# Optimization experiments

Hardware: AMD Instinct MI355X
Metric: run time of the kernel (lower is better)

The kernel has to match this reference:

```python
import jax, jax.numpy as jnp
import numpy as np

BIG = 1.0e9   # sentinel for masked distances / masked max
K_NBR = 64    # max_num_neighbors in radius()


def _fps(pos, n_sample):
    """Farthest point sampling on a single cloud pos [N, D] -> int32 [n_sample]."""
    n = pos.shape[0]

    def body(i, st):
        d, idxs = st
        last = pos[idxs[i - 1]]                              # [D]
        d = jnp.minimum(d, jnp.sum((pos - last) ** 2, axis=-1))
        return d, idxs.at[i].set(jnp.argmax(d).astype(jnp.int32))

    d0 = jnp.full((n,), BIG, pos.dtype)
    idxs0 = jnp.zeros((n_sample,), jnp.int32)
    _, idxs = jax.lax.fori_loop(1, n_sample, body, (d0, idxs0))
    return idxs


def _mlp2(h, w1, b1, w2, b2):
    # PyG MLP([a,b,c]) in eval mode (dropout off, batch-norm at default running
    # stats == identity): Linear -> ReLU -> Linear (plain last layer).
    return jax.nn.relu(h @ w1 + b1) @ w2 + b2


_gather = jax.vmap(lambda a, i: a[i])  # per-cloud fancy gather


def _sa(x, pos, ratio, r, w1, b1, w2, b2):
    """SAModule: FPS -> radius neighbors (<=K) -> PointConv (gather, MLP on
    [x_j, pos_j - pos_i], max-aggregate). Dense batched: x [B,N,C], pos [B,N,D]."""
    B, N, D = pos.shape
    M = int(round(N * ratio))
    idx = jax.vmap(lambda p: _fps(p, M))(pos)                 # [B, M]
    pos_q = _gather(pos, idx)                                 # [B, M, D]
    # pairwise squared distances query -> all points  [B, M, N]
    d2 = jnp.sum((pos_q[:, :, None, :] - pos[:, None, :, :]) ** 2, axis=-1)
    neg = jnp.where(d2 <= r * r, -d2, -BIG)
    vals, nbr = jax.lax.top_k(neg, K_NBR)                     # [B, M, K]
    valid = vals > -0.5 * BIG                                 # in-radius mask
    x_j = _gather(x, nbr)                                     # [B, M, K, C]
    rel = _gather(pos, nbr) - pos_q[:, :, None, :]            # [B, M, K, D]
    h = _mlp2(jnp.concatenate([x_j, rel], axis=-1), w1, b1, w2, b2)
    h = jnp.where(valid[..., None], h, -BIG)
    return jnp.max(h, axis=2), pos_q                          # max aggregation


def setup_inputs() -> dict:
    key = jax.random.key(0)
    ks = jax.random.split(key, 12)
    B, N, D, F = 8, 4096, 2, 5

    def lin(k, fi, fo):
        return (jax.random.normal(k, (fi, fo), jnp.float32) / np.sqrt(fi)).astype(jnp.float32)

    return {
        "x": jax.random.normal(ks[0], (B, N, F), jnp.float32),
        "pos": jax.random.uniform(ks[1], (B, N, D), jnp.float32),
        # sa1: MLP([5+2, 32, 64])
        "w1a": lin(ks[2], 7, 32),   "b1a": jnp.zeros((32,), jnp.float32),
        "w1b": lin(ks[3], 32, 64),  "b1b": jnp.zeros((64,), jnp.float32),
        # sa2: MLP([64+2, 64, 128])
        "w2a": lin(ks[4], 66, 64),  "b2a": jnp.zeros((64,), jnp.float32),
        "w2b": lin(ks[5], 64, 128), "b2b": jnp.zeros((128,), jnp.float32),
        # sa3 (global): MLP([128+2, 128, 256])
        "w3a": lin(ks[6], 130, 128), "b3a": jnp.zeros((128,), jnp.float32),
        "w3b": lin(ks[7], 128, 256), "b3b": jnp.zeros((256,), jnp.float32),
        # head: MLP([256, 256, 1024], norm=None)
        "w4a": lin(ks[8], 256, 256),  "b4a": jnp.zeros((256,), jnp.float32),
        "w4b": lin(ks[9], 256, 1024), "b4b": jnp.zeros((1024,), jnp.float32),
    }


def reference(x, pos, w1a, b1a, w1b, b1b, w2a, b2a, w2b, b2b,
              w3a, b3a, w3b, b3b, w4a, b4a, w4b, b4b):
    h1, p1 = _sa(x, pos, 0.5, 0.2, w1a, b1a, w1b, b1b)       # [B, N/2, 64]
    h2, p2 = _sa(h1, p1, 0.25, 0.4, w2a, b2a, w2b, b2b)      # [B, N/8, 128]
    g = _mlp2(jnp.concatenate([h2, p2], axis=-1), w3a, b3a, w3b, b3b)
    g = jnp.max(g, axis=1)                                    # global max pool [B, 256]
    return _mlp2(g, w4a, b4a, w4b, b4b)                       # [B, 1024]
```

## Files before the change

kernel.cpp:

```cpp
#include <hip/hip_runtime.h>


template<int N, int T>
__global__ __launch_bounds__(T) void fps_kernel(
    const float* __restrict__ pos,
    float* __restrict__ posq,
    int M) {
  constexpr int PPT = N / T;
  constexpr int NW  = T / 64;
  __shared__ float sx[N], sy[N];
  __shared__ unsigned long long sp[2][NW];
  const int b = blockIdx.x, t = threadIdx.x;
  const float* p = pos + (size_t)b * N * 2;
  float x[PPT], y[PPT], d[PPT];
  {
    const float4* p4 = (const float4*)(p + (size_t)t * PPT * 2);
#pragma unroll
    for (int q = 0; q < PPT / 2; ++q) {
      float4 v = p4[q];
      x[2 * q + 0] = v.x; y[2 * q + 0] = v.y;
      x[2 * q + 1] = v.z; y[2 * q + 1] = v.w;
    }
  }
#pragma unroll
  for (int k = 0; k < PPT; ++k) {
    int pt = t * PPT + k;
    sx[pt] = x[k]; sy[pt] = y[k];
    d[k] = 1e9f;
  }
  __syncthreads();
  float lx = sx[0], ly = sy[0];
  if (t == 0) { posq[(size_t)b * M * 2 + 0] = lx; posq[(size_t)b * M * 2 + 1] = ly; }

#define DPP_UMAX(u, ctrl)                                                      \
  do {                                                                         \
    unsigned _o = (unsigned)__builtin_amdgcn_update_dpp(0, (int)(u), (ctrl),   \
                                                        0xf, 0xf, true);       \
    (u) = ((u) > _o) ? (u) : _o;                                               \
  } while (0)

  for (int i = 1; i < M; ++i) {
    float bv = -1.0f; int bp = 0;
#pragma unroll
    for (int k = 0; k < PPT; ++k) {
      float dx = x[k] - lx, dy = y[k] - ly;
      float dd = __fadd_rn(__fmul_rn(dx, dx), __fmul_rn(dy, dy));
      float nd = fminf(d[k], dd);
      d[k] = nd;
      if (nd > bv) { bv = nd; bp = t * PPT + k; }
    }
    const unsigned mybits = __float_as_uint(bv);
    unsigned u = mybits;
    DPP_UMAX(u, 0x111);
    DPP_UMAX(u, 0x112);
    DPP_UMAX(u, 0x114);
    DPP_UMAX(u, 0x118);
    DPP_UMAX(u, 0x142);
    DPP_UMAX(u, 0x143);
    const unsigned wvb = (unsigned)__builtin_amdgcn_readlane((int)u, 63);
    const unsigned long long tm = __ballot(mybits == wvb);
    const int fl = (int)__builtin_ctzll(tm);
    const int wbp = __builtin_amdgcn_readlane(bp, fl);

    const int par = i & 1;
    if ((t & 63) == 0)
      sp[par][t >> 6] = ((unsigned long long)wvb << 32) | (unsigned)(~wbp);
    __syncthreads();
    unsigned long long best = sp[par][0];
#pragma unroll
    for (int j = 1; j < NW; ++j) {
      unsigned long long v = sp[par][j];
      best = (v > best) ? v : best;
    }
    const int wi = (int)(~(unsigned)best);
    lx = sx[wi]; ly = sy[wi];
    if (t == 0) {
      posq[((size_t)b * M + i) * 2 + 0] = lx;
      posq[((size_t)b * M + i) * 2 + 1] = ly;
    }
  }
#undef DPP_UMAX
}

template<int CPL>
__global__ __launch_bounds__(256) void nbr_kernel(
    const float* __restrict__ pts,
    const float* __restrict__ posq,
    int* __restrict__ nbr,
    int M, int NPTS, int total_q, float R2) {
  const int wid = blockIdx.x * 4 + (threadIdx.x >> 6);
  if (wid >= total_q) return;
  const int lane = threadIdx.x & 63;
  const int b = wid / M;
  const float qx = posq[(size_t)wid * 2 + 0], qy = posq[(size_t)wid * 2 + 1];
  const float* p = pts + (size_t)b * NPTS * 2;
  unsigned bits[CPL];
  int cnt = 0;
#pragma unroll
  for (int k = 0; k < CPL; ++k) {
    int pt = lane + (k << 6);
    float dx = p[pt * 2 + 0] - qx, dy = p[pt * 2 + 1] - qy;
    float dd = __fadd_rn(__fmul_rn(dx, dx), __fmul_rn(dy, dy));
    bool inr = (dd <= R2);
    bits[k] = inr ? __float_as_uint(dd) : 0xFFFFFFFFu;
    cnt += __popcll(__ballot(inr));
  }
  const unsigned long long below = (1ULL << lane) - 1ULL;
  if (cnt <= 64) {
    int base = 0;
#pragma unroll
    for (int k = 0; k < CPL; ++k) {
      bool s = (bits[k] != 0xFFFFFFFFu);
      unsigned long long m = __ballot(s);
      if (s) nbr[(size_t)wid * 64 + base + __popcll(m & below)] = lane + (k << 6);
      base += __popcll(m);
    }
    for (int j = base + lane; j < 64; j += 64) nbr[(size_t)wid * 64 + j] = -1;
  } else {
    unsigned lo = 0, hi = __float_as_uint(R2);
    while (lo < hi) {
      unsigned mid = lo + ((hi - lo) >> 1);
      int c = 0;
#pragma unroll
      for (int k = 0; k < CPL; ++k) c += __popcll(__ballot(bits[k] <= mid));
      if (c >= 64) hi = mid; else lo = mid + 1;
    }
    int cless = 0;
#pragma unroll
    for (int k = 0; k < CPL; ++k) cless += __popcll(__ballot(bits[k] < lo));
    const int need = 64 - cless;
    int base = 0, tiecnt = 0;
#pragma unroll
    for (int k = 0; k < CPL; ++k) {
      bool tie = (bits[k] == lo);
      unsigned long long tm = __ballot(tie);
      bool s = (bits[k] < lo) || (tie && (tiecnt + __popcll(tm & below)) < need);
      tiecnt += __popcll(tm);
      unsigned long long m = __ballot(s);
      if (s) nbr[(size_t)wid * 64 + base + __popcll(m & below)] = lane + (k << 6);
      base += __popcll(m);
    }
  }
}

template<int CIN, int H, int COUT, int QPB, int NPTS, int HS, int W1P>
__global__ __launch_bounds__(64 * QPB) void conv_kernel(
    const float* __restrict__ x,
    const float* __restrict__ pts,
    const float* __restrict__ posq,
    const int* __restrict__ nbr,
    const float* __restrict__ W1, const float* __restrict__ b1,
    const float* __restrict__ W2, const float* __restrict__ b2,
    float* __restrict__ out,
    int M) {
  constexpr int CI2 = CIN + 2;
  __shared__ float sW1t[H * W1P];
  __shared__ float sB1[H];
  __shared__ float sHH[QPB * 64 * HS];
  const int tid = threadIdx.x;
  for (int j = tid; j < CI2 * H; j += 64 * QPB) {
    int c = j / H, h = j - c * H;
    sW1t[h * W1P + c] = W1[j];
  }
  for (int j = tid; j < H; j += 64 * QPB) sB1[j] = b1[j];
  __syncthreads();
  const int wv = tid >> 6, lane = tid & 63;
  const int wid = blockIdx.x * QPB + wv;
  const int b = wid / M;
  const int idx = nbr[(size_t)wid * 64 + lane];
  const unsigned long long vm = __ballot(idx >= 0);
  const int ii = (idx < 0) ? 0 : idx;
  float in[CI2];
  {
    const float* xp = x + ((size_t)b * NPTS + ii) * CIN;
#pragma unroll
    for (int c = 0; c < CIN; ++c) in[c] = xp[c];
    float qx = posq[(size_t)wid * 2 + 0], qy = posq[(size_t)wid * 2 + 1];
    const float* pp = pts + ((size_t)b * NPTS + ii) * 2;
    in[CIN] = pp[0] - qx;
    in[CIN + 1] = pp[1] - qy;
  }
  float* hbase = &sHH[wv * 64 * HS];
#pragma unroll
  for (int h = 0; h < H; h += 4) {
    float vv[4];
#pragma unroll
    for (int j = 0; j < 4; ++j) {
      float a = sB1[h + j];
#pragma unroll
      for (int c = 0; c < CI2; ++c) a = fmaf(in[c], sW1t[(h + j) * W1P + c], a);
      vv[j] = fmaxf(a, 0.0f);
    }
    *(float4*)&hbase[lane * HS + h] = make_float4(vv[0], vv[1], vv[2], vv[3]);
  }
#pragma unroll
  for (int half = 0; half < COUT / 64; ++half) {
    const int o = half * 64 + lane;
    float w2r[H];
#pragma unroll
    for (int h = 0; h < H; ++h) w2r[h] = W2[h * COUT + o];
    const float b2o = b2[o];
    float m = -1e30f;
    for (int n = 0; n < 64; ++n) {
      const float4* hp = (const float4*)&hbase[n * HS];
      float a = b2o;
#pragma unroll
      for (int j = 0; j < H / 4; ++j) {
        float4 hv = hp[j];
        a = fmaf(hv.x, w2r[4 * j + 0], a);
        a = fmaf(hv.y, w2r[4 * j + 1], a);
        a = fmaf(hv.z, w2r[4 * j + 2], a);
        a = fmaf(hv.w, w2r[4 * j + 3], a);
      }
      a = ((vm >> n) & 1ULL) ? a : -1e9f;
      m = fmaxf(m, a);
    }
    out[(size_t)wid * COUT + o] = m;
  }
}

__global__ __launch_bounds__(256) void u_kernel(
    const float* __restrict__ h2,
    const float* __restrict__ posq2,
    const float* __restrict__ W3a, const float* __restrict__ b3a,
    float* __restrict__ u) {
  const int p = blockIdx.x * 2 + (threadIdx.x >> 7);
  const int h = threadIdx.x & 127;
  const float* hp = h2 + (size_t)p * 128;
  float a = b3a[h];
  for (int c = 0; c < 128; ++c) a = fmaf(hp[c], W3a[c * 128 + h], a);
  a = fmaf(posq2[(size_t)p * 2 + 0], W3a[128 * 128 + h], a);
  a = fmaf(posq2[(size_t)p * 2 + 1], W3a[129 * 128 + h], a);
  u[(size_t)p * 128 + h] = fmaxf(a, 0.0f);
}

__global__ __launch_bounds__(256) void g_kernel(
    const float* __restrict__ u,
    const float* __restrict__ W3b, const float* __restrict__ b3b,
    float* __restrict__ part) {
  __shared__ float su[64 * 128];
  const int bb = blockIdx.x;
  const float* up = u + (size_t)bb * 64 * 128;
  for (int j = threadIdx.x; j < 64 * 128; j += 256) su[j] = up[j];
  __syncthreads();
  const int o = threadIdx.x;
  float w[128];
#pragma unroll
  for (int h = 0; h < 128; ++h) w[h] = W3b[h * 256 + o];
  float m = -1e30f;
  for (int p = 0; p < 64; ++p) {
    float a = b3b[o];
    const float4* sp = (const float4*)&su[p * 128];
#pragma unroll
    for (int j = 0; j < 32; ++j) {
      float4 v = sp[j];
      a = fmaf(v.x, w[4 * j + 0], a);
      a = fmaf(v.y, w[4 * j + 1], a);
      a = fmaf(v.z, w[4 * j + 2], a);
      a = fmaf(v.w, w[4 * j + 3], a);
    }
    m = fmaxf(m, a);
  }
  part[(size_t)bb * 256 + o] = m;
}

__global__ __launch_bounds__(256) void head_kernel(
    const float* __restrict__ part,
    const float* __restrict__ W4a, const float* __restrict__ b4a,
    const float* __restrict__ W4b, const float* __restrict__ b4b,
    float* __restrict__ out) {
  __shared__ float g[256], h4[256];
  const int b = blockIdx.x, t = threadIdx.x;
  float m = part[(size_t)(b * 8 + 0) * 256 + t];
  for (int c = 1; c < 8; ++c) m = fmaxf(m, part[(size_t)(b * 8 + c) * 256 + t]);
  g[t] = m;
  __syncthreads();
  float a = b4a[t];
  for (int c = 0; c < 256; ++c) a = fmaf(g[c], W4a[c * 256 + t], a);
  h4[t] = fmaxf(a, 0.0f);
  __syncthreads();
  for (int jj = 0; jj < 4; ++jj) {
    int o = t + jj * 256;
    float a2 = b4b[o];
    for (int c = 0; c < 256; ++c) a2 = fmaf(h4[c], W4b[c * 1024 + o], a2);
    out[(size_t)b * 1024 + o] = a2;
  }
}

extern "C" void kernel_launch(void* const* d_in, const int* in_sizes, int n_in,
                              void* d_out, int out_size, void* d_ws, size_t ws_size,
                              hipStream_t stream) {
  (void)in_sizes; (void)n_in; (void)out_size; (void)ws_size;
  const float* x   = (const float*)d_in[0];
  const float* pos = (const float*)d_in[1];
  const float* w1a = (const float*)d_in[2];  const float* b1a = (const float*)d_in[3];
  const float* w1b = (const float*)d_in[4];  const float* b1b = (const float*)d_in[5];
  const float* w2a = (const float*)d_in[6];  const float* b2a = (const float*)d_in[7];
  const float* w2b = (const float*)d_in[8];  const float* b2b = (const float*)d_in[9];
  const float* w3a = (const float*)d_in[10]; const float* b3a = (const float*)d_in[11];
  const float* w3b = (const float*)d_in[12]; const float* b3b = (const float*)d_in[13];
  const float* w4a = (const float*)d_in[14]; const float* b4a = (const float*)d_in[15];
  const float* w4b = (const float*)d_in[16]; const float* b4b = (const float*)d_in[17];
  float* outp = (float*)d_out;

  char* ws = (char*)d_ws;
  size_t off = 0;
  float* posq1 = (float*)(ws + off); off += (size_t)8 * 2048 * 2 * 4;
  float* posq2 = (float*)(ws + off); off += (size_t)8 * 512 * 2 * 4;
  int*   nbr1  = (int*)  (ws + off); off += (size_t)16384 * 64 * 4;
  int*   nbr2  = (int*)  (ws + off); off += (size_t)4096 * 64 * 4;
  float* h1    = (float*)(ws + off); off += (size_t)16384 * 64 * 4;
  float* h2    = (float*)(ws + off); off += (size_t)4096 * 128 * 4;
  float* u3    = (float*)(ws + off); off += (size_t)4096 * 128 * 4;
  float* part  = (float*)(ws + off); off += (size_t)64 * 256 * 4;

  fps_kernel<4096, 512><<<dim3(8), dim3(512), 0, stream>>>(pos, posq1, 2048);
  fps_kernel<2048, 512><<<dim3(8), dim3(512), 0, stream>>>(posq1, posq2, 512);
  nbr_kernel<64><<<dim3(4096), dim3(256), 0, stream>>>(pos, posq1, nbr1,
                                                       2048, 4096, 16384, 0.04f);
  conv_kernel<5, 32, 64, 4, 4096, 36, 8><<<dim3(4096), dim3(256), 0, stream>>>(
      x, pos, posq1, nbr1, w1a, b1a, w1b, b1b, h1, 2048);
  nbr_kernel<32><<<dim3(1024), dim3(256), 0, stream>>>(posq1, posq2, nbr2,
                                                       512, 2048, 4096, 0.16f);
  conv_kernel<64, 64, 128, 2, 2048, 68, 68><<<dim3(2048), dim3(128), 0, stream>>>(
      h1, posq1, posq2, nbr2, w2a, b2a, w2b, b2b, h2, 512);
  u_kernel<<<dim3(2048), dim3(256), 0, stream>>>(h2, posq2, w3a, b3a, u3);
  g_kernel<<<dim3(64), dim3(256), 0, stream>>>(u3, w3b, b3b, part);
  head_kernel<<<dim3(8), dim3(256), 0, stream>>>(part, w4a, b4a, w4b, b4b, outp);
}
```

Baseline: 1.995 ms.

## Fuse both FPS stages into one kernel and carry winner coordinates in reduction slots

Runs both farthest-point-sampling stages in a single kernel, keeping the sampled points in shared memory so the second stage skips a kernel launch and a global round trip. The winning point's coordinates now travel with its key in the per-wave shared slots and are picked out of registers with a select tree, which removes the dependent shared-memory lookup of the winner after each barrier. The per-thread argmax is split into two interleaved chains to shorten the dependency chain. The cost is more registers for the coordinate copies and a wider uint4 slot reduction done by every thread.

```diff
diff --git a/kernel.cpp b/kernel.cpp
--- a/kernel.cpp
+++ b/kernel.cpp
@@ -1,36 +1,5 @@
 #include <hip/hip_runtime.h>
 
-
-template<int N, int T>
-__global__ __launch_bounds__(T) void fps_kernel(
-    const float* __restrict__ pos,
-    float* __restrict__ posq,
-    int M) {
-  constexpr int PPT = N / T;
-  constexpr int NW  = T / 64;
-  __shared__ float sx[N], sy[N];
-  __shared__ unsigned long long sp[2][NW];
-  const int b = blockIdx.x, t = threadIdx.x;
-  const float* p = pos + (size_t)b * N * 2;
-  float x[PPT], y[PPT], d[PPT];
-  {
-    const float4* p4 = (const float4*)(p + (size_t)t * PPT * 2);
-#pragma unroll
-    for (int q = 0; q < PPT / 2; ++q) {
-      float4 v = p4[q];
-      x[2 * q + 0] = v.x; y[2 * q + 0] = v.y;
-      x[2 * q + 1] = v.z; y[2 * q + 1] = v.w;
-    }
-  }
-#pragma unroll
-  for (int k = 0; k < PPT; ++k) {
-    int pt = t * PPT + k;
-    sx[pt] = x[k]; sy[pt] = y[k];
-    d[k] = 1e9f;
-  }
-  __syncthreads();
-  float lx = sx[0], ly = sy[0];
-  if (t == 0) { posq[(size_t)b * M * 2 + 0] = lx; posq[(size_t)b * M * 2 + 1] = ly; }
 
 #define DPP_UMAX(u, ctrl)                                                      \
   do {                                                                         \
@@ -39,15 +8,58 @@
     (u) = ((u) > _o) ? (u) : _o;                                               \
   } while (0)
 
-  for (int i = 1; i < M; ++i) {
-    float bv = -1.0f; int bp = 0;
+__device__ __forceinline__ uint4 kmax4(uint4 a, uint4 b) {
+  unsigned long long ka = ((unsigned long long)a.y << 32) | a.x;
+  unsigned long long kb = ((unsigned long long)b.y << 32) | b.x;
+  bool c = kb > ka;
+  uint4 r;
+  r.x = c ? b.x : a.x; r.y = c ? b.y : a.y;
+  r.z = c ? b.z : a.z; r.w = c ? b.w : a.w;
+  return r;
+}
+
+template<int PPT, int T>
+__device__ __forceinline__ void fps_stage(
+    float (&xr)[PPT], float (&yr)[PPT], int Msel, int t,
+    float* wlx, float* wly, uint4* slots ) {
+  constexpr int NW = T / 64;
+  if (t == 0) { wlx[0] = xr[0]; wly[0] = yr[0]; }
+  __syncthreads();
+  float lx = wlx[0], ly = wly[0];
+  float d[PPT];
+#pragma unroll
+  for (int k = 0; k < PPT; ++k) d[k] = 1e9f;
+
+  for (int i = 1; i < Msel; ++i) {
+    float nd[PPT];
 #pragma unroll
     for (int k = 0; k < PPT; ++k) {
-      float dx = x[k] - lx, dy = y[k] - ly;
+      float dx = xr[k] - lx, dy = yr[k] - ly;
       float dd = __fadd_rn(__fmul_rn(dx, dx), __fmul_rn(dy, dy));
-      float nd = fminf(d[k], dd);
-      d[k] = nd;
-      if (nd > bv) { bv = nd; bp = t * PPT + k; }
+      float v = fminf(d[k], dd);
+      d[k] = v; nd[k] = v;
+    }
+    constexpr int HP = PPT / 2;
+    float bvA = nd[0]; int bkA = 0;
+    float bvB = nd[HP]; int bkB = HP;
+#pragma unroll
+    for (int k = 1; k < HP; ++k) {
+      if (nd[k] > bvA)      { bvA = nd[k];      bkA = k; }
+      if (nd[HP + k] > bvB) { bvB = nd[HP + k]; bkB = HP + k; }
+    }
+    float bv = bvA; int bk = bkA;
+    if (bvB > bvA) { bv = bvB; bk = bkB; }
+    float tx[PPT], ty[PPT];
+#pragma unroll
+    for (int k = 0; k < PPT; ++k) { tx[k] = xr[k]; ty[k] = yr[k]; }
+#pragma unroll
+    for (int s = 1; s < PPT; s <<= 1) {
+      bool c = (bk & s) != 0;
+#pragma unroll
+      for (int k = 0; k < PPT; k += 2 * s) {
+        tx[k] = c ? tx[k + s] : tx[k];
+        ty[k] = c ? ty[k + s] : ty[k];
+      }
     }
     const unsigned mybits = __float_as_uint(bv);
     unsigned u = mybits;
@@ -58,28 +70,63 @@
     DPP_UMAX(u, 0x142);
     DPP_UMAX(u, 0x143);
     const unsigned wvb = (unsigned)__builtin_amdgcn_readlane((int)u, 63);
-    const unsigned long long tm = __ballot(mybits == wvb);
-    const int fl = (int)__builtin_ctzll(tm);
-    const int wbp = __builtin_amdgcn_readlane(bp, fl);
-
+    const unsigned long long tmask = __ballot(mybits == wvb);
+    const int fl = (int)__builtin_ctzll(tmask);
     const int par = i & 1;
-    if ((t & 63) == 0)
-      sp[par][t >> 6] = ((unsigned long long)wvb << 32) | (unsigned)(~wbp);
+    if ((t & 63) == fl) {
+      uint4 s4;
+      s4.x = ~(unsigned)(t * PPT + bk);
+      s4.y = wvb;
+      s4.z = __float_as_uint(tx[0]);
+      s4.w = __float_as_uint(ty[0]);
+      slots[par * NW + (t >> 6)] = s4;
+    }
     __syncthreads();
-    unsigned long long best = sp[par][0];
-#pragma unroll
-    for (int j = 1; j < NW; ++j) {
-      unsigned long long v = sp[par][j];
-      best = (v > best) ? v : best;
-    }
-    const int wi = (int)(~(unsigned)best);
-    lx = sx[wi]; ly = sy[wi];
-    if (t == 0) {
-      posq[((size_t)b * M + i) * 2 + 0] = lx;
-      posq[((size_t)b * M + i) * 2 + 1] = ly;
-    }
-  }
-#undef DPP_UMAX
+    const uint4* sl = &slots[par * NW];
+    uint4 arr[NW];
+#pragma unroll
+    for (int j = 0; j < NW; ++j) arr[j] = sl[j];
+#pragma unroll
+    for (int s = NW / 2; s >= 1; s >>= 1)
+#pragma unroll
+      for (int j = 0; j < s; ++j) arr[j] = kmax4(arr[j], arr[j + s]);
+    lx = __uint_as_float(arr[0].z);
+    ly = __uint_as_float(arr[0].w);
+    if (t == 0) { wlx[i] = lx; wly[i] = ly; }
+  }
+}
+
+template<int N, int M1, int M2, int T>
+__global__ __launch_bounds__(T) void fps_fused_kernel(
+    const float* __restrict__ pos,
+    float* __restrict__ posq1,
+    float* __restrict__ posq2) {
+  constexpr int PPT  = N / T;
+  constexpr int PPT2 = M1 / T;
+  constexpr int NW   = T / 64;
+  __shared__ float wlx[M1], wly[M1];
+  __shared__ uint4 slots[2 * NW];
+  const int b = blockIdx.x, t = threadIdx.x;
+  float xr[PPT], yr[PPT];
+  const float4* p4 = (const float4*)(pos + (size_t)b * N * 2 + (size_t)t * PPT * 2);
+#pragma unroll
+  for (int q = 0; q < PPT / 2; ++q) {
+    float4 v = p4[q];
+    xr[2 * q + 0] = v.x; yr[2 * q + 0] = v.y;
+    xr[2 * q + 1] = v.z; yr[2 * q + 1] = v.w;
+  }
+  fps_stage<PPT, T>(xr, yr, M1, t, wlx, wly, slots);
+  __syncthreads();
+  for (int j = t; j < M1; j += T)
+    ((float2*)posq1)[(size_t)b * M1 + j] = make_float2(wlx[j], wly[j]);
+  float x2[PPT2], y2[PPT2];
+#pragma unroll
+  for (int k = 0; k < PPT2; ++k) { x2[k] = wlx[t * PPT2 + k]; y2[k] = wly[t * PPT2 + k]; }
+  __syncthreads();
+  fps_stage<PPT2, T>(x2, y2, M2, t, wlx, wly, slots);
+  __syncthreads();
+  for (int j = t; j < M2; j += T)
+    ((float2*)posq2)[(size_t)b * M2 + j] = make_float2(wlx[j], wly[j]);
 }
 
 template<int CPL>
@@ -314,8 +361,8 @@
   float* u3    = (float*)(ws + off); off += (size_t)4096 * 128 * 4;
   float* part  = (float*)(ws + off); off += (size_t)64 * 256 * 4;
 
-  fps_kernel<4096, 512><<<dim3(8), dim3(512), 0, stream>>>(pos, posq1, 2048);
-  fps_kernel<2048, 512><<<dim3(8), dim3(512), 0, stream>>>(posq1, posq2, 512);
+  fps_fused_kernel<4096, 2048, 512, 512><<<dim3(8), dim3(512), 0, stream>>>(
+      pos, posq1, posq2);
   nbr_kernel<64><<<dim3(4096), dim3(256), 0, stream>>>(pos, posq1, nbr1,
                                                        2048, 4096, 16384, 0.04f);
   conv_kernel<5, 32, 64, 4, 4096, 36, 8><<<dim3(4096), dim3(256), 0, stream>>>(
```

New measurement: 4.825 ms. +141.8%, slower.
